# Performance work log

Hardware: AMD Instinct MI355X
Metric: run time of the kernel (lower is better)

Reference implementation:

```python
import jax, jax.numpy as jnp
import numpy as np

B, L, C, H, W = 4, 4096, 1024, 16, 512
D = C // H            # head_dim = 64
STRIDE = W // 2


def setup_inputs() -> dict:
    key = jax.random.key(0)
    k0, k1, k2 = jax.random.split(key, 3)
    s = 0.02
    return {
        "x": jax.random.normal(k0, (B, L, C), jnp.float32),
        "w_qkv": jax.random.normal(k1, (C, 3 * C), jnp.float32) * s,
        "b_qkv": jnp.zeros((3 * C,), jnp.float32),
        "w_out": jax.random.normal(k2, (C, C), jnp.float32) * s,
        "b_out": jnp.zeros((C,), jnp.float32),
    }


def _local_attention(x, w_qkv, b_qkv, w_out, b_out):
    b, l, c = x.shape
    pad = (-l) % W  # pad seq to multiple of window_size (0 here)
    x = jnp.pad(x, ((0, 0), (0, pad), (0, 0)))
    lp = l + pad
    qkv = (x @ w_qkv + b_qkv).reshape(b, lp, 3, H, D).transpose(2, 0, 3, 1, 4)
    q, k, v = qkv[0], qkv[1], qkv[2]  # each [B, H, Lp, D]
    nw = (lp - W) // STRIDE + 1       # number of overlapping windows
    # window token indices [nw, W]
    idx = jnp.arange(nw)[:, None] * STRIDE + jnp.arange(W)[None, :]
    qw = q[:, :, idx, :]  # [B, H, nw, W, D]
    kw = k[:, :, idx, :]
    vw = v[:, :, idx, :]
    # non-causal (bidirectional=True) attention within each window,
    # flash-attn default softmax scale = head_dim**-0.5
    scores = jnp.einsum('bhnqd,bhnkd->bhnqk', qw, kw) / jnp.sqrt(jnp.float32(D))
    probs = jax.nn.softmax(scores, axis=-1)
    ow = jnp.einsum('bhnqk,bhnkd->bhnqd', probs, vw)  # [B, H, nw, W, D]
    # concatenate window outputs along sequence, back to [B, nw*W, C]
    o = ow.transpose(0, 2, 3, 1, 4).reshape(b, nw * W, c)
    o = o @ w_out + b_out
    return o[:, :l, :]


def reference(x, w_qkv, b_qkv, w_out, b_out):
    return _local_attention(x, w_qkv, b_qkv, w_out, b_out)
```

## Files before the change

kernel.cpp:

```cpp
#include <hip/hip_runtime.h>

#define LQ 2304

typedef __attribute__((ext_vector_type(8))) short bf16x8;
typedef __attribute__((ext_vector_type(8))) unsigned short u16x8;
typedef __attribute__((ext_vector_type(4))) float f32x4;

#define MFMA(a, b, c) __builtin_amdgcn_mfma_f32_16x16x32_bf16((a), (b), (c), 0, 0, 0)
#define AS1 __attribute__((address_space(1)))
#define AS3 __attribute__((address_space(3)))

static __device__ __forceinline__ unsigned short f2bf(float f) {
  unsigned int u = __builtin_bit_cast(unsigned int, f);
  u += 0x7fffu + ((u >> 16) & 1u);
  return (unsigned short)(u >> 16);
}

static __device__ __forceinline__ void lds16(const unsigned short* g, unsigned short* l) {
  __builtin_amdgcn_global_load_lds((AS1 const unsigned int*)g, (AS3 unsigned int*)l, 16, 0, 0);
}

__global__ __launch_bounds__(256) void conv_x(const float* __restrict__ x,
                                              unsigned short* __restrict__ xbf) {
  int b = blockIdx.y;
  int g = blockIdx.x * 256 + threadIdx.x;
  int row = g >> 7, c8 = (g & 127) * 8;
  const float* src = x + ((size_t)b * 4096 + row) * 1024 + c8;
  float4 f0 = *(const float4*)src;
  float4 f1 = *(const float4*)(src + 4);
  u16x8 u;
  u[0] = f2bf(f0.x); u[1] = f2bf(f0.y); u[2] = f2bf(f0.z); u[3] = f2bf(f0.w);
  u[4] = f2bf(f1.x); u[5] = f2bf(f1.y); u[6] = f2bf(f1.z); u[7] = f2bf(f1.w);
  *(u16x8*)(xbf + ((size_t)b * 2304 + row) * 1024 + c8) = u;
}

__global__ __launch_bounds__(256) void transpose_conv(const float* __restrict__ src,
                                                      unsigned short* __restrict__ dst,
                                                      int K, int N) {
  __shared__ float t[32][33];
  int bn = blockIdx.x * 32, bk = blockIdx.y * 32;
  int tx = threadIdx.x, ty = threadIdx.y;
  for (int i = ty; i < 32; i += 8)
    t[i][tx] = src[(size_t)(bk + i) * N + bn + tx];
  __syncthreads();
  for (int i = ty; i < 32; i += 8)
    dst[(size_t)(bn + i) * K + bk + tx] = f2bf(t[tx][i]);
}

#define K2SCALE 0.18033688011112042f
__global__ __launch_bounds__(256) void qkv_gemm(const unsigned short* __restrict__ xbf,
                                                const float* __restrict__ bqkv,
                                                const unsigned short* __restrict__ wT,
                                                unsigned short* __restrict__ qws,
                                                unsigned short* __restrict__ kws,
                                                unsigned short* __restrict__ vws) {
  __shared__ __align__(16) unsigned short As[128 * 32];
  __shared__ __align__(16) unsigned short Bs[128 * 32];
  const int tid = threadIdx.x;
  const int mt = blockIdx.y;
  const int nt = blockIdx.x;
  const int bidx = mt / 18;
  const int l0 = (mt % 18) * 128;
  const int n0 = nt * 128;
  const int lane = tid & 63, wv = tid >> 6;
  const int wm = (wv >> 1) * 64, wn = (wv & 1) * 64;
  const int l16 = lane & 15, quad = lane >> 4;

  const unsigned short* ga = xbf + ((size_t)bidx * LQ + l0 + wv * 32 + (lane >> 2)) * 1024 + (lane & 3) * 8;
  const unsigned short* gb = wT + (size_t)(n0 + wv * 32 + (lane >> 2)) * 1024 + (lane & 3) * 8;
  unsigned short* la = As + wv * 1024;
  unsigned short* lb = Bs + wv * 1024;

  const f32x4 zero4 = {0.f, 0.f, 0.f, 0.f};
  f32x4 acc[4][4];
#pragma unroll
  for (int i = 0; i < 4; i++)
#pragma unroll
    for (int j = 0; j < 4; j++) acc[i][j] = zero4;

  for (int k0 = 0; k0 < 1024; k0 += 32) {
    __syncthreads();
    lds16(ga, la);
    lds16(ga + 16 * 1024, la + 512);
    lds16(gb, lb);
    lds16(gb + 16 * 1024, lb + 512);
    __syncthreads();
    bf16x8 af[4], bfv[4];
#pragma unroll
    for (int i = 0; i < 4; i++)
      af[i] = *(const bf16x8*)(&As[(wm + i * 16 + l16) * 32 + quad * 8]);
#pragma unroll
    for (int j = 0; j < 4; j++)
      bfv[j] = *(const bf16x8*)(&Bs[(wn + j * 16 + l16) * 32 + quad * 8]);
#pragma unroll
    for (int i = 0; i < 4; i++)
#pragma unroll
      for (int j = 0; j < 4; j++)
        acc[i][j] = MFMA(af[i], bfv[j], acc[i][j]);
    ga += 32;
    gb += 32;
  }

#pragma unroll
  for (int j = 0; j < 4; j++) {
    int col = n0 + wn + j * 16 + l16;
    int which = col >> 10;
    int hcol = (col >> 6) & 15;
    int dcol = col & 63;
    unsigned short* dst = which == 0 ? qws : (which == 1 ? kws : vws);
    float scale = which == 0 ? K2SCALE : 1.0f;
    float bias = bqkv[col];
    size_t cbase = ((size_t)bidx * 16 + hcol) * LQ * 64 + dcol;
#pragma unroll
    for (int i = 0; i < 4; i++) {
      int lrow = l0 + wm + i * 16 + quad * 4;
#pragma unroll
      for (int r = 0; r < 4; r++)
        dst[cbase + (size_t)(lrow + r) * 64] = f2bf((acc[i][j][r] + bias) * scale);
    }
  }
}

#define KSTR 72
#define VSTR 520
#define ATTN_LDS ((512 * KSTR + 64 * VSTR) * 2)

__global__ __launch_bounds__(512) void attn_kernel(const unsigned short* __restrict__ q,
                                                   const unsigned short* __restrict__ k,
                                                   const unsigned short* __restrict__ v,
                                                   unsigned short* __restrict__ o) {
  extern __shared__ unsigned short lds[];
  unsigned short* Ks = lds;
  unsigned short* Vt = lds + 512 * KSTR;
  const int n = blockIdx.x, h = blockIdx.y, b = blockIdx.z;
  const size_t base = (((size_t)b * 16 + h) * LQ + n * 256) * 64;
  const unsigned short* qg = q + base;
  const unsigned short* kg = k + base;
  const unsigned short* vg = v + base;
  const int tid = threadIdx.x;

  for (int i = tid; i < 4096; i += 512) {
    int key = i >> 3, part = i & 7;
    *(u16x8*)(&Ks[key * KSTR + part * 8]) = *(const u16x8*)(kg + (size_t)key * 64 + part * 8);
  }
  for (int i = tid; i < 4096; i += 512) {
    int key = i >> 3, part = i & 7;
    u16x8 raw = *(const u16x8*)(vg + (size_t)key * 64 + part * 8);
    int pos = (key & ~31) + ((key >> 2) & 3) * 8 + ((key >> 4) & 1) * 4 + (key & 3);
    int d0 = part * 8;
#pragma unroll
    for (int t = 0; t < 8; t++) Vt[(d0 + t) * VSTR + pos] = raw[t];
  }
  __syncthreads();

  const int lane = tid & 63, wv = tid >> 6;
  const int l16 = lane & 15, quad = lane >> 4;
  const f32x4 zero4 = {0.f, 0.f, 0.f, 0.f};

  for (int qs = 0; qs < 4; qs++) {
    int qrow = wv * 64 + qs * 16 + l16;
    bf16x8 qf0 = *(const bf16x8*)(qg + (size_t)qrow * 64 + quad * 8);
    bf16x8 qf1 = *(const bf16x8*)(qg + (size_t)qrow * 64 + quad * 8 + 32);
    f32x4 O[4];
#pragma unroll
    for (int dt = 0; dt < 4; dt++) O[dt] = zero4;
    float lsum = 0.f;

    for (int c = 0; c < 16; c++) {
      f32x4 s0 = zero4, s1 = zero4;
      const unsigned short* kr0 = &Ks[(c * 32 + l16) * KSTR + quad * 8];
      s0 = MFMA(*(const bf16x8*)kr0, qf0, s0);
      s0 = MFMA(*(const bf16x8*)(kr0 + 32), qf1, s0);
      const unsigned short* kr1 = kr0 + 16 * KSTR;
      s1 = MFMA(*(const bf16x8*)kr1, qf0, s1);
      s1 = MFMA(*(const bf16x8*)(kr1 + 32), qf1, s1);
      bf16x8 pf;
#pragma unroll
      for (int r = 0; r < 4; r++) {
        float p0 = __builtin_amdgcn_exp2f(s0[r]);
        float p1 = __builtin_amdgcn_exp2f(s1[r]);
        lsum += p0 + p1;
        pf[r] = (short)f2bf(p0);
        pf[4 + r] = (short)f2bf(p1);
      }
#pragma unroll
      for (int dt = 0; dt < 4; dt++) {
        bf16x8 vf = *(const bf16x8*)(&Vt[(dt * 16 + l16) * VSTR + c * 32 + quad * 8]);
        O[dt] = MFMA(pf, vf, O[dt]);
      }
    }
    lsum += __shfl_xor(lsum, 16);
    lsum += __shfl_xor(lsum, 32);
    float linv = 1.0f / lsum;
    float li[4];
#pragma unroll
    for (int r = 0; r < 4; r++) li[r] = __shfl(linv, quad * 4 + r);
    size_t orow = (size_t)b * 4096 + n * 512 + wv * 64 + qs * 16;
#pragma unroll
    for (int dt = 0; dt < 4; dt++) {
      int col = h * 64 + dt * 16 + l16;
#pragma unroll
      for (int r = 0; r < 4; r++)
        o[(orow + quad * 4 + r) * 1024 + col] = f2bf(O[dt][r] * li[r]);
    }
  }
}

__global__ __launch_bounds__(256) void out_gemm(const unsigned short* __restrict__ A,
                                                const unsigned short* __restrict__ wT,
                                                const float* __restrict__ bout,
                                                float* __restrict__ out) {
  __shared__ __align__(16) unsigned short As[128 * 32];
  __shared__ __align__(16) unsigned short Bs[128 * 32];
  const int tid = threadIdx.x;
  const int m0 = blockIdx.y * 128;
  const int n0 = blockIdx.x * 128;
  const int lane = tid & 63, wv = tid >> 6;
  const int wm = (wv >> 1) * 64, wn = (wv & 1) * 64;
  const int l16 = lane & 15, quad = lane >> 4;

  const unsigned short* ga = A + (size_t)(m0 + wv * 32 + (lane >> 2)) * 1024 + (lane & 3) * 8;
  const unsigned short* gb = wT + (size_t)(n0 + wv * 32 + (lane >> 2)) * 1024 + (lane & 3) * 8;
  unsigned short* la = As + wv * 1024;
  unsigned short* lb = Bs + wv * 1024;

  const f32x4 zero4 = {0.f, 0.f, 0.f, 0.f};
  f32x4 acc[4][4];
#pragma unroll
  for (int i = 0; i < 4; i++)
#pragma unroll
    for (int j = 0; j < 4; j++) acc[i][j] = zero4;

  for (int k0 = 0; k0 < 1024; k0 += 32) {
    __syncthreads();
    lds16(ga, la);
    lds16(ga + 16 * 1024, la + 512);
    lds16(gb, lb);
    lds16(gb + 16 * 1024, lb + 512);
    __syncthreads();
    bf16x8 af[4], bfv[4];
#pragma unroll
    for (int i = 0; i < 4; i++)
      af[i] = *(const bf16x8*)(&As[(wm + i * 16 + l16) * 32 + quad * 8]);
#pragma unroll
    for (int j = 0; j < 4; j++)
      bfv[j] = *(const bf16x8*)(&Bs[(wn + j * 16 + l16) * 32 + quad * 8]);
#pragma unroll
    for (int i = 0; i < 4; i++)
#pragma unroll
      for (int j = 0; j < 4; j++)
        acc[i][j] = MFMA(af[i], bfv[j], acc[i][j]);
    ga += 32;
    gb += 32;
  }

#pragma unroll
  for (int j = 0; j < 4; j++) {
    int col = n0 + wn + j * 16 + l16;
    float bias = bout[col];
#pragma unroll
    for (int i = 0; i < 4; i++) {
      int row = m0 + wm + i * 16 + quad * 4;
#pragma unroll
      for (int r = 0; r < 4; r++)
        out[(size_t)(row + r) * 1024 + col] = acc[i][j][r] + bias;
    }
  }
}

#define WQKVT_OFF 0u
#define WOUTT_OFF (WQKVT_OFF + 3072u * 1024u * 2u)
#define QWS_OFF   (WOUTT_OFF + 1024u * 1024u * 2u)
#define KVQ_SZ    (4u * 16u * 2304u * 64u * 2u)
#define KWS_OFF   (QWS_OFF + KVQ_SZ)
#define VWS_OFF   (KWS_OFF + KVQ_SZ)
#define OWS_OFF   (VWS_OFF + KVQ_SZ)
#define XBF_OFF   OWS_OFF

extern "C" void kernel_launch(void* const* d_in, const int* in_sizes, int n_in,
                              void* d_out, int out_size, void* d_ws, size_t ws_size,
                              hipStream_t stream) {
  const float* x     = (const float*)d_in[0];
  const float* w_qkv = (const float*)d_in[1];
  const float* b_qkv = (const float*)d_in[2];
  const float* w_out = (const float*)d_in[3];
  const float* b_out = (const float*)d_in[4];
  float* out = (float*)d_out;
  char* ws = (char*)d_ws;

  unsigned short* wqkvT = (unsigned short*)(ws + WQKVT_OFF);
  unsigned short* woutT = (unsigned short*)(ws + WOUTT_OFF);
  unsigned short* qws   = (unsigned short*)(ws + QWS_OFF);
  unsigned short* kws   = (unsigned short*)(ws + KWS_OFF);
  unsigned short* vws   = (unsigned short*)(ws + VWS_OFF);
  unsigned short* ows   = (unsigned short*)(ws + OWS_OFF);
  unsigned short* xbf   = (unsigned short*)(ws + XBF_OFF);

  conv_x<<<dim3(1152, 4), 256, 0, stream>>>(x, xbf);
  transpose_conv<<<dim3(96, 32), dim3(32, 8), 0, stream>>>(w_qkv, wqkvT, 1024, 3072);
  transpose_conv<<<dim3(32, 32), dim3(32, 8), 0, stream>>>(w_out, woutT, 1024, 1024);

  qkv_gemm<<<dim3(24, 72), 256, 0, stream>>>(xbf, b_qkv, wqkvT, qws, kws, vws);

  (void)hipFuncSetAttribute((const void*)attn_kernel,
                            hipFuncAttributeMaxDynamicSharedMemorySize, ATTN_LDS);
  attn_kernel<<<dim3(8, 16, 4), 512, ATTN_LDS, stream>>>(qws, kws, vws, ows);

  out_gemm<<<dim3(8, 128), 256, 0, stream>>>(ows, woutT, b_out, out);
}
```

Baseline: 339.2 us.

## Reuse K/V LDS fragments across four query subtiles in attention loop

Restructures the attention inner loop so each wave loads its K and V fragments from LDS once per key chunk and applies them to all four 16-row query subtiles, instead of reloading them for every subtile. Q fragments and the O accumulators for all subtiles now stay in registers, and the launch bound requests two blocks per CU. The change also replaces the rounding bf16 conversion of the probabilities with a truncating byte-permute pack, adding a small bias to the exponent to offset the truncation. It remaps the V transpose load so each wave handles fixed columns. The tradeoffs are higher register pressure and slightly different rounding.

```diff
diff --git a/kernel.cpp b/kernel.cpp
--- a/kernel.cpp
+++ b/kernel.cpp
@@ -5,6 +5,7 @@
 typedef __attribute__((ext_vector_type(8))) short bf16x8;
 typedef __attribute__((ext_vector_type(8))) unsigned short u16x8;
 typedef __attribute__((ext_vector_type(4))) float f32x4;
+typedef __attribute__((ext_vector_type(4))) unsigned int u32x4;
 
 #define MFMA(a, b, c) __builtin_amdgcn_mfma_f32_16x16x32_bf16((a), (b), (c), 0, 0, 0)
 #define AS1 __attribute__((address_space(1)))
@@ -14,6 +15,11 @@
   unsigned int u = __builtin_bit_cast(unsigned int, f);
   u += 0x7fffu + ((u >> 16) & 1u);
   return (unsigned short)(u >> 16);
+}
+
+static __device__ __forceinline__ unsigned int pkbf(float hi, float lo) {
+  return __builtin_amdgcn_perm(__builtin_bit_cast(unsigned int, hi),
+                               __builtin_bit_cast(unsigned int, lo), 0x07060302u);
 }
 
 static __device__ __forceinline__ void lds16(const unsigned short* g, unsigned short* l) {
@@ -125,10 +131,10 @@
 #define VSTR 520
 #define ATTN_LDS ((512 * KSTR + 64 * VSTR) * 2)
 
-__global__ __launch_bounds__(512) void attn_kernel(const unsigned short* __restrict__ q,
-                                                   const unsigned short* __restrict__ k,
-                                                   const unsigned short* __restrict__ v,
-                                                   unsigned short* __restrict__ o) {
+__global__ __launch_bounds__(512, 2) void attn_kernel(const unsigned short* __restrict__ q,
+                                                      const unsigned short* __restrict__ k,
+                                                      const unsigned short* __restrict__ v,
+                                                      unsigned short* __restrict__ o) {
   extern __shared__ unsigned short lds[];
   unsigned short* Ks = lds;
   unsigned short* Vt = lds + 512 * KSTR;
@@ -138,60 +144,82 @@
   const unsigned short* kg = k + base;
   const unsigned short* vg = v + base;
   const int tid = threadIdx.x;
+  const int lane = tid & 63, wv = tid >> 6;
 
   for (int i = tid; i < 4096; i += 512) {
     int key = i >> 3, part = i & 7;
     *(u16x8*)(&Ks[key * KSTR + part * 8]) = *(const u16x8*)(kg + (size_t)key * 64 + part * 8);
   }
-  for (int i = tid; i < 4096; i += 512) {
-    int key = i >> 3, part = i & 7;
-    u16x8 raw = *(const u16x8*)(vg + (size_t)key * 64 + part * 8);
+  for (int it = 0; it < 8; it++) {
+    int key = it * 64 + lane;
+    u16x8 raw = *(const u16x8*)(vg + (size_t)key * 64 + wv * 8);
     int pos = (key & ~31) + ((key >> 2) & 3) * 8 + ((key >> 4) & 1) * 4 + (key & 3);
-    int d0 = part * 8;
-#pragma unroll
-    for (int t = 0; t < 8; t++) Vt[(d0 + t) * VSTR + pos] = raw[t];
+#pragma unroll
+    for (int t = 0; t < 8; t++) Vt[(wv * 8 + t) * VSTR + pos] = raw[t];
   }
   __syncthreads();
 
-  const int lane = tid & 63, wv = tid >> 6;
   const int l16 = lane & 15, quad = lane >> 4;
   const f32x4 zero4 = {0.f, 0.f, 0.f, 0.f};
-
+  const float RB = 0.002815015607053277f;
+
+  bf16x8 qf0[4], qf1[4];
+#pragma unroll
   for (int qs = 0; qs < 4; qs++) {
     int qrow = wv * 64 + qs * 16 + l16;
-    bf16x8 qf0 = *(const bf16x8*)(qg + (size_t)qrow * 64 + quad * 8);
-    bf16x8 qf1 = *(const bf16x8*)(qg + (size_t)qrow * 64 + quad * 8 + 32);
-    f32x4 O[4];
-#pragma unroll
-    for (int dt = 0; dt < 4; dt++) O[dt] = zero4;
-    float lsum = 0.f;
-
-    for (int c = 0; c < 16; c++) {
+    qf0[qs] = *(const bf16x8*)(qg + (size_t)qrow * 64 + quad * 8);
+    qf1[qs] = *(const bf16x8*)(qg + (size_t)qrow * 64 + quad * 8 + 32);
+  }
+  f32x4 O[4][4];
+#pragma unroll
+  for (int qs = 0; qs < 4; qs++)
+#pragma unroll
+    for (int dt = 0; dt < 4; dt++) O[qs][dt] = zero4;
+  float lsum[4] = {0.f, 0.f, 0.f, 0.f};
+
+  for (int c = 0; c < 16; c++) {
+    const unsigned short* kr0 = &Ks[(c * 32 + l16) * KSTR + quad * 8];
+    bf16x8 ka0 = *(const bf16x8*)kr0;
+    bf16x8 ka1 = *(const bf16x8*)(kr0 + 32);
+    bf16x8 kb0 = *(const bf16x8*)(kr0 + 16 * KSTR);
+    bf16x8 kb1 = *(const bf16x8*)(kr0 + 16 * KSTR + 32);
+    bf16x8 vf[4];
+#pragma unroll
+    for (int dt = 0; dt < 4; dt++)
+      vf[dt] = *(const bf16x8*)(&Vt[(dt * 16 + l16) * VSTR + c * 32 + quad * 8]);
+#pragma unroll
+    for (int qs = 0; qs < 4; qs++) {
       f32x4 s0 = zero4, s1 = zero4;
-      const unsigned short* kr0 = &Ks[(c * 32 + l16) * KSTR + quad * 8];
-      s0 = MFMA(*(const bf16x8*)kr0, qf0, s0);
-      s0 = MFMA(*(const bf16x8*)(kr0 + 32), qf1, s0);
-      const unsigned short* kr1 = kr0 + 16 * KSTR;
-      s1 = MFMA(*(const bf16x8*)kr1, qf0, s1);
-      s1 = MFMA(*(const bf16x8*)(kr1 + 32), qf1, s1);
-      bf16x8 pf;
+      s0 = MFMA(ka0, qf0[qs], s0);
+      s0 = MFMA(ka1, qf1[qs], s0);
+      s1 = MFMA(kb0, qf0[qs], s1);
+      s1 = MFMA(kb1, qf1[qs], s1);
+      float p0[4], p1[4], ls = 0.f;
 #pragma unroll
       for (int r = 0; r < 4; r++) {
-        float p0 = __builtin_amdgcn_exp2f(s0[r]);
-        float p1 = __builtin_amdgcn_exp2f(s1[r]);
-        lsum += p0 + p1;
-        pf[r] = (short)f2bf(p0);
-        pf[4 + r] = (short)f2bf(p1);
+        p0[r] = __builtin_amdgcn_exp2f(s0[r] + RB);
+        p1[r] = __builtin_amdgcn_exp2f(s1[r] + RB);
+        ls += p0[r] + p1[r];
       }
-#pragma unroll
-      for (int dt = 0; dt < 4; dt++) {
-        bf16x8 vf = *(const bf16x8*)(&Vt[(dt * 16 + l16) * VSTR + c * 32 + quad * 8]);
-        O[dt] = MFMA(pf, vf, O[dt]);
-      }
+      lsum[qs] += ls;
+      u32x4 pw;
+      pw[0] = pkbf(p0[1], p0[0]);
+      pw[1] = pkbf(p0[3], p0[2]);
+      pw[2] = pkbf(p1[1], p1[0]);
+      pw[3] = pkbf(p1[3], p1[2]);
+      bf16x8 pf = __builtin_bit_cast(bf16x8, pw);
+#pragma unroll
+      for (int dt = 0; dt < 4; dt++)
+        O[qs][dt] = MFMA(pf, vf[dt], O[qs][dt]);
     }
-    lsum += __shfl_xor(lsum, 16);
-    lsum += __shfl_xor(lsum, 32);
-    float linv = 1.0f / lsum;
+  }
+
+#pragma unroll
+  for (int qs = 0; qs < 4; qs++) {
+    float ls = lsum[qs];
+    ls += __shfl_xor(ls, 16);
+    ls += __shfl_xor(ls, 32);
+    float linv = 1.0f / ls;
     float li[4];
 #pragma unroll
     for (int r = 0; r < 4; r++) li[r] = __shfl(linv, quad * 4 + r);
@@ -201,7 +229,7 @@
       int col = h * 64 + dt * 16 + l16;
 #pragma unroll
       for (int r = 0; r < 4; r++)
-        o[(orow + quad * 4 + r) * 1024 + col] = f2bf(O[dt][r] * li[r]);
+        o[(orow + quad * 4 + r) * 1024 + col] = f2bf(O[qs][dt][r] * li[r]);
     }
   }
 }
```

Result: faster. 330.2 us (-2.7%).
